# Performance work log

Hardware: AMD Instinct MI355X
Metric: run time of the kernel (lower is better)

## Reference

```python
import jax, jax.numpy as jnp
import numpy as np

MAX_POS = 1024  # config.max_position_embeddings
NUM_HEADS = 16
HEAD_DIM = 64


def setup_inputs() -> dict:
    key = jax.random.key(0)
    ks = jax.random.split(key, 4)
    B, S, H = 4, 1024, 1024
    return {
        "hidden_states": jax.random.normal(ks[0], (B, S, H), dtype=jnp.float32),
        "qkv_w": jax.random.normal(ks[1], (3 * H, H), dtype=jnp.float32) * 0.02,
        "qkv_b": jax.random.normal(ks[2], (3 * H,), dtype=jnp.float32) * 0.02,
        "dist_emb": jax.random.normal(ks[3], (2 * MAX_POS - 1, HEAD_DIM), dtype=jnp.float32) * 0.02,
        "ext_mask": jnp.zeros((B, 1, 1, S), dtype=jnp.float32),
    }


def reference(hidden_states, qkv_w, qkv_b, dist_emb, ext_mask):
    B, S, H = hidden_states.shape
    h, d = NUM_HEADS, HEAD_DIM
    # fused QKV projection (q|k|v concatenated on output dim)
    qkv = jnp.einsum('bsi,oi->bso', hidden_states, qkv_w) + qkv_b
    q, k, v = jnp.split(qkv, 3, axis=-1)
    to_heads = lambda x: x.reshape(B, S, h, d).transpose(0, 2, 1, 3)  # [B,h,S,d]
    q, k, v = to_heads(q), to_heads(k), to_heads(v)
    # raw attention scores [B,h,S,S]
    scores = jnp.einsum('bhld,bhrd->bhlr', q, k)
    # relative_key_query positional bias
    pos = jnp.arange(S)
    distance = pos[:, None] - pos[None, :]          # [S,S]
    pe = dist_emb[distance + MAX_POS - 1]           # [S,S,d]
    scores = scores + jnp.einsum('bhld,lrd->bhlr', q, pe) \
                    + jnp.einsum('bhrd,lrd->bhlr', k, pe)
    scores = scores / jnp.sqrt(jnp.asarray(d, scores.dtype))
    scores = scores + ext_mask
    probs = jax.nn.softmax(scores, axis=-1)
    ctx = jnp.einsum('bhlr,bhrd->bhld', probs, v)   # [B,h,S,d]
    return ctx.transpose(0, 2, 1, 3).reshape(B, S, h * d)
```

## Files before the change

### kernel.cpp

```cpp
#include <hip/hip_runtime.h>

#define SEQ 1024
#define NH  16

typedef __attribute__((ext_vector_type(8))) short short8;
typedef __attribute__((ext_vector_type(4))) float floatx4;
typedef __attribute__((ext_vector_type(4))) unsigned short ushortx4;

#define GLDS16(gp, lp) __builtin_amdgcn_global_load_lds( \
    (const __attribute__((address_space(1))) void*)(gp), \
    (__attribute__((address_space(3))) void*)(lp), 16, 0, 0)

__device__ __forceinline__ unsigned short f2b(float f) {
    union { float f; unsigned u; } v; v.f = f;
    unsigned r = (v.u + 0x7fffu + ((v.u >> 16) & 1u)) >> 16;
    return (unsigned short)r;
}
__device__ __forceinline__ float b2f(unsigned short h) {
    union { unsigned u; float f; } v; v.u = ((unsigned)h) << 16;
    return v.f;
}

#define TADDR(base, row, ch) ((base) + ((row) << 6) + ((((ch) ^ ((row) & 7))) << 3))

__global__ void cast_kernel(const float* __restrict__ hs, const float* __restrict__ W,
                            const float* __restrict__ E,
                            unsigned short* __restrict__ hsb,
                            unsigned short* __restrict__ Wb,
                            unsigned short* __restrict__ Eb)
{
    const int QH = 1048576, QW = 786432, QE = 32752;
    const int NT = QH + QW + QE;
    for (int q = blockIdx.x * 256 + threadIdx.x; q < NT; q += gridDim.x * 256) {
        const float* src; unsigned short* dst; int off;
        if (q < QH)           { src = hs; dst = hsb; off = q; }
        else if (q < QH + QW) { src = W;  dst = Wb;  off = q - QH; }
        else                  { src = E;  dst = Eb;  off = q - QH - QW; }
        const float4 v = *(const float4*)(src + (size_t)off * 4);
        ushortx4 o; o[0] = f2b(v.x); o[1] = f2b(v.y); o[2] = f2b(v.z); o[3] = f2b(v.w);
        *(ushortx4*)(dst + (size_t)off * 4) = o;
    }
}

__global__ __launch_bounds__(256, 3) void qkv_gemm(
    const unsigned short* __restrict__ Ab, const unsigned short* __restrict__ Bb,
    const float* __restrict__ bias,
    unsigned short* __restrict__ Qb, unsigned short* __restrict__ Kb,
    unsigned short* __restrict__ Vt)
{
    __shared__ unsigned short sm[8192];
    const int t = threadIdx.x, w = t >> 6;
    const int ln = t & 15, g = (t >> 4) & 3;
    const int wm = w >> 1, wn = w & 1;
    const int m0 = blockIdx.y << 7, o0 = blockIdx.x << 7;

    floatx4 acc[4][4];
#pragma unroll
    for (int i = 0; i < 4; ++i)
#pragma unroll
        for (int j = 0; j < 4; ++j) acc[i][j] = (floatx4){0.f, 0.f, 0.f, 0.f};

    auto stage = [&](int kb) {
#pragma unroll
        for (int p = 0; p < 2; ++p) {
            const int idx = (p << 8) + t;
            const int row = idx >> 2;
            const int c = (idx & 3) ^ ((row ^ (row >> 2)) & 3);
            GLDS16(Ab + (size_t)(m0 + row) * 1024 + kb + (c << 3),
                   (char*)sm + (p << 12) + (w << 10));
            GLDS16(Bb + (size_t)(o0 + row) * 1024 + kb + (c << 3),
                   (char*)sm + 8192 + (p << 12) + (w << 10));
        }
    };

    stage(0);
    for (int kb = 0;;) {
        __syncthreads();
        short8 af[4], bf_[4];
#pragma unroll
        for (int i = 0; i < 4; ++i) {
            const int r = (wm << 6) + (i << 4) + ln;
            af[i] = *(const short8*)&sm[(r << 5) + ((g ^ ((r ^ (r >> 2)) & 3)) << 3)];
        }
#pragma unroll
        for (int j = 0; j < 4; ++j) {
            const int r = (wn << 6) + (j << 4) + ln;
            bf_[j] = *(const short8*)&sm[4096 + (r << 5) + ((g ^ ((r ^ (r >> 2)) & 3)) << 3)];
        }
#pragma unroll
        for (int i = 0; i < 4; ++i)
#pragma unroll
            for (int j = 0; j < 4; ++j)
                acc[i][j] = __builtin_amdgcn_mfma_f32_16x16x32_bf16(af[i], bf_[j], acc[i][j], 0, 0, 0);
        kb += 32;
        if (kb >= 1024) break;
        __syncthreads();
        stage(kb);
    }

    const int which = o0 >> 10;
    float bj[4];
#pragma unroll
    for (int j = 0; j < 4; ++j) bj[j] = bias[o0 + (wn << 6) + (j << 4) + ln];

    if (which == 2) {
#pragma unroll
        for (int i = 0; i < 4; ++i) {
            const int m = m0 + (wm << 6) + (i << 4) + (g << 2);
            const int b = m >> 10, s = m & 1023;
#pragma unroll
            for (int j = 0; j < 4; ++j) {
                const int o = o0 + (wn << 6) + (j << 4) + ln;
                const int d = o & 63, hh = (o >> 6) & 15;
                ushortx4 pk;
#pragma unroll
                for (int q = 0; q < 4; ++q) pk[q] = f2b(acc[i][j][q] + bj[j]);
                *(ushortx4*)(Vt + (((size_t)((b << 4) + hh)) << 16) + (d << 10) + s) = pk;
            }
        }
    } else {
        unsigned short* dst = which ? Kb : Qb;
        const float sc = which ? 1.0f : 0.125f;
#pragma unroll
        for (int i = 0; i < 4; ++i)
#pragma unroll
            for (int q = 0; q < 4; ++q) {
                const int m = m0 + (wm << 6) + (i << 4) + (g << 2) + q;
                const int b = m >> 10, s = m & 1023;
#pragma unroll
                for (int j = 0; j < 4; ++j) {
                    const int o = o0 + (wn << 6) + (j << 4) + ln;
                    const int d = o & 63, hh = (o >> 6) & 15;
                    dst[(((size_t)((b << 4) + hh)) << 16) + (s << 6) + d] =
                        f2b((acc[i][j][q] + bj[j]) * sc);
                }
            }
    }
}

__global__ __launch_bounds__(256, 3) void attn_mfma(
    const unsigned short* __restrict__ Qb, const unsigned short* __restrict__ Kb,
    const unsigned short* __restrict__ Vt, const unsigned short* __restrict__ Eb,
    const float* __restrict__ mask, float* __restrict__ outp)
{
    __shared__ __align__(16) unsigned short sm[25600];
    const int t = threadIdx.x, w = t >> 6;
    const int wu = __builtin_amdgcn_readfirstlane(w);
    const int ln = t & 15, g = (t >> 4) & 3;
    const int bid = blockIdx.x;
    const int swz = ((bid & 7) << 7) | (bid >> 3);
    const int bh = swz >> 4;
    const int l0 = (swz & 15) << 6;
    const int b = bh >> 4, h = bh & 15;
    const size_t hb = (size_t)bh << 16;
    const int x0 = (w << 4) + (g << 2);

    const int qr = (w << 4) + ln;
    const short8 qa0 = *(const short8*)(Qb + hb + ((size_t)(l0 + qr) << 6) + (g << 3));
    const short8 qa1 = *(const short8*)(Qb + hb + ((size_t)(l0 + qr) << 6) + 32 + (g << 3));

    floatx4 O[4];
    float mr[4], lr[4];
#pragma unroll
    for (int dt = 0; dt < 4; ++dt) O[dt] = (floatx4){0.f, 0.f, 0.f, 0.f};
#pragma unroll
    for (int q = 0; q < 4; ++q) { mr[q] = -1e30f; lr[q] = 0.f; }

    for (int r0 = 0; r0 < SEQ; r0 += 64) {
        __syncthreads();
#pragma unroll
        for (int p = 0; p < 2; ++p) {
            const int idx = (p << 8) + t;
            const int row = idx >> 3;
            const int c = (idx & 7) ^ (row & 7);
            GLDS16(Kb + hb + ((size_t)(r0 + row) << 6) + (c << 3),
                   (char*)sm + (p << 12) + (w << 10));
        }
        const int j0 = l0 - r0 + 960;
#pragma unroll
        for (int p = 0; p < 4; ++p) {
            const int idx = (p << 8) + t;
            const int row = idx >> 3;
            const int c = (idx & 7) ^ (row & 7);
            GLDS16(Eb + ((size_t)(j0 + row) << 6) + (c << 3),
                   (char*)sm + 8192 + (p << 12) + (w << 10));
        }
        __syncthreads();
        short8 kf[4][2];
#pragma unroll
        for (int j = 0; j < 4; ++j) {
            const int kr = (j << 4) + ln;
            kf[j][0] = *(const short8*)&sm[TADDR(0, kr, g)];
            kf[j][1] = *(const short8*)&sm[TADDR(0, kr, 4 + g)];
        }
        const int wr = (w << 4) + ln;
        const short8 ka0 = *(const short8*)&sm[TADDR(0, wr, g)];
        const short8 ka1 = *(const short8*)&sm[TADDR(0, wr, 4 + g)];

        floatx4 S[4];
#pragma unroll
        for (int j = 0; j < 4; ++j) {
            floatx4 z = (floatx4){0.f, 0.f, 0.f, 0.f};
            z = __builtin_amdgcn_mfma_f32_16x16x32_bf16(qa0, kf[j][0], z, 0, 0, 0);
            S[j] = __builtin_amdgcn_mfma_f32_16x16x32_bf16(qa1, kf[j][1], z, 0, 0, 0);
        }
#pragma unroll
        for (int dt = 0; dt < 8; ++dt) {
            const bool doU = (dt >= wu) && (dt <= wu + 4);
            const bool doW = (dt >= 3 - wu) && (dt <= 7 - wu);
            if (!doU && !doW) continue;
            const int er = (dt << 4) + ln;
            const short8 e0 = *(const short8*)&sm[TADDR(4096, er, g)];
            const short8 e1 = *(const short8*)&sm[TADDR(4096, er, 4 + g)];
            if (doU) {
                floatx4 z = (floatx4){0.f, 0.f, 0.f, 0.f};
                z = __builtin_amdgcn_mfma_f32_16x16x32_bf16(qa0, e0, z, 0, 0, 0);
                const floatx4 U = __builtin_amdgcn_mfma_f32_16x16x32_bf16(qa1, e1, z, 0, 0, 0);
                int a = 12288 + (x0 - (dt << 4) - ln + 79) * 72 + x0;
#pragma unroll
                for (int q = 0; q < 4; ++q) { sm[a] = f2b(U[q]); a += 73; }
            }
            if (doW) {
                floatx4 z2 = (floatx4){0.f, 0.f, 0.f, 0.f};
                z2 = __builtin_amdgcn_mfma_f32_16x16x32_bf16(ka0, e0, z2, 0, 0, 0);
                const floatx4 Wv = __builtin_amdgcn_mfma_f32_16x16x32_bf16(ka1, e1, z2, 0, 0, 0);
                int a = 19200 + x0 * 101 + (dt << 4) + ln - 47;
#pragma unroll
                for (int q = 0; q < 4; ++q) { sm[a] = f2b(Wv[q] * 0.125f); a += 101; }
            }
        }
        __syncthreads();
#pragma unroll
        for (int p = 0; p < 2; ++p) {
            const int idx = (p << 8) + t;
            const int row = idx >> 3;
            const int c = (idx & 7) ^ (row & 7);
            GLDS16(Vt + hb + ((size_t)row << 10) + r0 + (c << 3),
                   (char*)sm + 8192 + (p << 12) + (w << 10));
        }
        float Pw[4][4];
#pragma unroll
        for (int j = 0; j < 4; ++j) {
            const int rr = (j << 4) + ln;
            const float mk = mask[(b << 10) + r0 + rr];
            const ushortx4 u4 = *(const ushortx4*)&sm[12288 + (rr + 16) * 72 + x0];
            const ushortx4 w4 = *(const ushortx4*)&sm[19200 + rr * 100 + 16 + x0];
#pragma unroll
            for (int q = 0; q < 4; ++q)
                S[j][q] += b2f(u4[q]) + b2f(w4[q]) + mk;
        }
#pragma unroll
        for (int q = 0; q < 4; ++q) {
            float tm = fmaxf(fmaxf(S[0][q], S[1][q]), fmaxf(S[2][q], S[3][q]));
            tm = fmaxf(tm, __shfl_xor(tm, 1));
            tm = fmaxf(tm, __shfl_xor(tm, 2));
            tm = fmaxf(tm, __shfl_xor(tm, 4));
            tm = fmaxf(tm, __shfl_xor(tm, 8));
            const float mnew = fmaxf(mr[q], tm);
            const float al = __expf(mr[q] - mnew);
            float sum = 0.f;
#pragma unroll
            for (int j = 0; j < 4; ++j) {
                const float p = __expf(S[j][q] - mnew);
                Pw[j][q] = p; sum += p;
            }
            sum += __shfl_xor(sum, 1);
            sum += __shfl_xor(sum, 2);
            sum += __shfl_xor(sum, 4);
            sum += __shfl_xor(sum, 8);
            lr[q] = lr[q] * al + sum;
            mr[q] = mnew;
#pragma unroll
            for (int dt = 0; dt < 4; ++dt) O[dt][q] *= al;
        }
#pragma unroll
        for (int j = 0; j < 4; ++j) {
            const int rr = (j << 4) + ln;
#pragma unroll
            for (int q = 0; q < 4; ++q) {
                const int l = x0 + q;
                sm[8192 + (l << 6) + ((((rr >> 3) ^ (l & 7)) << 3)) + (rr & 7)] = f2b(Pw[j][q]);
            }
        }
        __syncthreads();
        const int pr = (w << 4) + ln;
        const short8 pa0 = *(const short8*)&sm[TADDR(8192, pr, g)];
        const short8 pa1 = *(const short8*)&sm[TADDR(8192, pr, 4 + g)];
#pragma unroll
        for (int dt = 0; dt < 4; ++dt) {
            const int vr = (dt << 4) + ln;
            const short8 v0 = *(const short8*)&sm[TADDR(4096, vr, g)];
            const short8 v1 = *(const short8*)&sm[TADDR(4096, vr, 4 + g)];
            O[dt] = __builtin_amdgcn_mfma_f32_16x16x32_bf16(pa0, v0, O[dt], 0, 0, 0);
            O[dt] = __builtin_amdgcn_mfma_f32_16x16x32_bf16(pa1, v1, O[dt], 0, 0, 0);
        }
    }
#pragma unroll
    for (int dt = 0; dt < 4; ++dt)
#pragma unroll
        for (int q = 0; q < 4; ++q) {
            const int l = x0 + q;
            outp[((size_t)b << 20) + ((size_t)(l0 + l) << 10) + (h << 6) + (dt << 4) + ln]
                = O[dt][q] / lr[q];
        }
}

extern "C" void kernel_launch(void* const* d_in, const int* in_sizes, int n_in,
                              void* d_out, int out_size, void* d_ws, size_t ws_size,
                              hipStream_t stream)
{
    const float* hs   = (const float*)d_in[0];
    const float* qkvw = (const float*)d_in[1];
    const float* qkvb = (const float*)d_in[2];
    const float* demb = (const float*)d_in[3];
    const float* mask = (const float*)d_in[4];
    float* out = (float*)d_out;

    char* ws = (char*)d_ws;
    unsigned short* hsb = (unsigned short*)(ws);
    unsigned short* Wb  = (unsigned short*)(ws + 8388608);
    unsigned short* Eb  = (unsigned short*)(ws + 14680064);
    unsigned short* Qb  = (unsigned short*)(ws + 14942208);
    unsigned short* Kb  = (unsigned short*)(ws + 23330816);
    unsigned short* Vt  = (unsigned short*)(ws + 31719424);

    cast_kernel<<<2048, 256, 0, stream>>>(hs, qkvw, demb, hsb, Wb, Eb);
    qkv_gemm<<<dim3(24, 32), 256, 0, stream>>>(hsb, Wb, qkvb, Qb, Kb, Vt);
    attn_mfma<<<1024, 256, 0, stream>>>(Qb, Kb, Vt, Eb, mask, out);
}
```

Measured before the change: 230.2 us.

## Double-buffer QKV GEMM, swizzle its tile order, hoist mask loads, add MFMA priority hints

```diff
diff --git a/kernel.cpp b/kernel.cpp
--- a/kernel.cpp
+++ b/kernel.cpp
@@ -48,11 +48,13 @@
     unsigned short* __restrict__ Qb, unsigned short* __restrict__ Kb,
     unsigned short* __restrict__ Vt)
 {
-    __shared__ unsigned short sm[8192];
+    __shared__ unsigned short sm[16384];
     const int t = threadIdx.x, w = t >> 6;
     const int ln = t & 15, g = (t >> 4) & 3;
     const int wm = w >> 1, wn = w & 1;
-    const int m0 = blockIdx.y << 7, o0 = blockIdx.x << 7;
+    const int bid = blockIdx.x + blockIdx.y * 24;
+    const int swzid = (bid & 7) * 96 + (bid >> 3);
+    const int m0 = (swzid / 24) << 7, o0 = (swzid % 24) << 7;
 
     floatx4 acc[4][4];
 #pragma unroll
@@ -60,42 +62,44 @@
 #pragma unroll
         for (int j = 0; j < 4; ++j) acc[i][j] = (floatx4){0.f, 0.f, 0.f, 0.f};
 
-    auto stage = [&](int kb) {
+    auto stage = [&](int kb, int buf) {
+        const int base = buf << 14;
 #pragma unroll
         for (int p = 0; p < 2; ++p) {
             const int idx = (p << 8) + t;
             const int row = idx >> 2;
             const int c = (idx & 3) ^ ((row ^ (row >> 2)) & 3);
             GLDS16(Ab + (size_t)(m0 + row) * 1024 + kb + (c << 3),
-                   (char*)sm + (p << 12) + (w << 10));
+                   (char*)sm + base + (p << 12) + (w << 10));
             GLDS16(Bb + (size_t)(o0 + row) * 1024 + kb + (c << 3),
-                   (char*)sm + 8192 + (p << 12) + (w << 10));
+                   (char*)sm + base + 8192 + (p << 12) + (w << 10));
         }
     };
 
-    stage(0);
-    for (int kb = 0;;) {
-        __syncthreads();
+    stage(0, 0);
+    __syncthreads();
+    int buf = 0;
+    for (int kb = 0; kb < 1024; kb += 32) {
+        if (kb + 32 < 1024) stage(kb + 32, buf ^ 1);
+        const int be = buf << 13;
         short8 af[4], bf_[4];
 #pragma unroll
         for (int i = 0; i < 4; ++i) {
             const int r = (wm << 6) + (i << 4) + ln;
-            af[i] = *(const short8*)&sm[(r << 5) + ((g ^ ((r ^ (r >> 2)) & 3)) << 3)];
+            af[i] = *(const short8*)&sm[be + (r << 5) + ((g ^ ((r ^ (r >> 2)) & 3)) << 3)];
         }
 #pragma unroll
         for (int j = 0; j < 4; ++j) {
             const int r = (wn << 6) + (j << 4) + ln;
-            bf_[j] = *(const short8*)&sm[4096 + (r << 5) + ((g ^ ((r ^ (r >> 2)) & 3)) << 3)];
+            bf_[j] = *(const short8*)&sm[be + 4096 + (r << 5) + ((g ^ ((r ^ (r >> 2)) & 3)) << 3)];
         }
 #pragma unroll
         for (int i = 0; i < 4; ++i)
 #pragma unroll
             for (int j = 0; j < 4; ++j)
                 acc[i][j] = __builtin_amdgcn_mfma_f32_16x16x32_bf16(af[i], bf_[j], acc[i][j], 0, 0, 0);
-        kb += 32;
-        if (kb >= 1024) break;
-        __syncthreads();
-        stage(kb);
+        __syncthreads();
+        buf ^= 1;
     }
 
     const int which = o0 >> 10;
@@ -167,6 +171,10 @@
     for (int q = 0; q < 4; ++q) { mr[q] = -1e30f; lr[q] = 0.f; }
 
     for (int r0 = 0; r0 < SEQ; r0 += 64) {
+        float mk4[4];
+#pragma unroll
+        for (int j = 0; j < 4; ++j) mk4[j] = mask[(b << 10) + r0 + (j << 4) + ln];
+
         __syncthreads();
 #pragma unroll
         for (int p = 0; p < 2; ++p) {
@@ -197,6 +205,7 @@
         const short8 ka0 = *(const short8*)&sm[TADDR(0, wr, g)];
         const short8 ka1 = *(const short8*)&sm[TADDR(0, wr, 4 + g)];
 
+        __builtin_amdgcn_s_setprio(1);
         floatx4 S[4];
 #pragma unroll
         for (int j = 0; j < 4; ++j) {
@@ -229,6 +238,7 @@
                 for (int q = 0; q < 4; ++q) { sm[a] = f2b(Wv[q] * 0.125f); a += 101; }
             }
         }
+        __builtin_amdgcn_s_setprio(0);
         __syncthreads();
 #pragma unroll
         for (int p = 0; p < 2; ++p) {
@@ -242,12 +252,11 @@
 #pragma unroll
         for (int j = 0; j < 4; ++j) {
             const int rr = (j << 4) + ln;
-            const float mk = mask[(b << 10) + r0 + rr];
             const ushortx4 u4 = *(const ushortx4*)&sm[12288 + (rr + 16) * 72 + x0];
             const ushortx4 w4 = *(const ushortx4*)&sm[19200 + rr * 100 + 16 + x0];
 #pragma unroll
             for (int q = 0; q < 4; ++q)
-                S[j][q] += b2f(u4[q]) + b2f(w4[q]) + mk;
+                S[j][q] += b2f(u4[q]) + b2f(w4[q]) + mk4[j];
         }
 #pragma unroll
         for (int q = 0; q < 4; ++q) {
@@ -286,6 +295,7 @@
         const int pr = (w << 4) + ln;
         const short8 pa0 = *(const short8*)&sm[TADDR(8192, pr, g)];
         const short8 pa1 = *(const short8*)&sm[TADDR(8192, pr, 4 + g)];
+        __builtin_amdgcn_s_setprio(1);
 #pragma unroll
         for (int dt = 0; dt < 4; ++dt) {
             const int vr = (dt << 4) + ln;
@@ -294,6 +304,7 @@
             O[dt] = __builtin_amdgcn_mfma_f32_16x16x32_bf16(pa0, v0, O[dt], 0, 0, 0);
             O[dt] = __builtin_amdgcn_mfma_f32_16x16x32_bf16(pa1, v1, O[dt], 0, 0, 0);
         }
+        __builtin_amdgcn_s_setprio(0);
     }
 #pragma unroll
     for (int dt = 0; dt < 4; ++dt)
```

Measured after the change: 234.5 us. No clear change (+1.9%).
